# Performance work log

Hardware: AMD Instinct MI355X
Metric: run time of the kernel (lower is better)

The kernel has to match this reference:

```python
import jax, jax.numpy as jnp
import numpy as np

THETA_BASE = 10000.0


def _rope_tables(head_dim, seq_len):
    # intended math of precompute_rope_params (source has an arange typo;
    # standard RoPE: inv_freq over even indices)
    inv_freq = 1.0 / (THETA_BASE ** (jnp.arange(0, head_dim, 2, dtype=jnp.float32) / head_dim))
    pos = jnp.arange(seq_len, dtype=jnp.float32)
    angles = pos[:, None] * inv_freq[None, :]          # [S, hd/2]
    angles = jnp.concatenate([angles, angles], axis=1)  # [S, hd]
    return jnp.cos(angles), jnp.sin(angles)


def _apply_rope(x, cos, sin):
    # x: [B, H, S, hd]; cos/sin: [S, hd] broadcast over batch/heads
    hd = x.shape[-1]
    x1, x2 = x[..., : hd // 2], x[..., hd // 2 :]
    rotated = jnp.concatenate([-x2, x1], axis=-1)
    return x * cos + rotated * sin


def setup_inputs() -> dict:
    key = jax.random.key(0)
    ks = jax.random.split(key, 5)
    b, s, d = 2, 2048, 1024
    x = jax.random.normal(ks[0], (b, s, d), dtype=jnp.float32)
    # store weights as [d_in, d_out] so y = x @ W (equivalent math to nn.Linear)
    scale = 1.0 / np.sqrt(d)
    W_q = jax.random.normal(ks[1], (d, d), dtype=jnp.float32) * scale
    W_k = jax.random.normal(ks[2], (d, d), dtype=jnp.float32) * scale
    W_v = jax.random.normal(ks[3], (d, d), dtype=jnp.float32) * scale
    W_o = jax.random.normal(ks[4], (d, d), dtype=jnp.float32) * scale
    return {"x": x, "W_q": W_q, "W_k": W_k, "W_v": W_v, "W_o": W_o}


def reference(x, W_q, W_k, W_v, W_o):
    num_heads = 16
    b, s, d_in = x.shape
    d_out = W_q.shape[1]
    hd = d_out // num_heads

    def split_heads(t):  # [B,S,D] -> [B,H,S,hd]
        return t.reshape(b, s, num_heads, hd).transpose(0, 2, 1, 3)

    q = split_heads(x @ W_q)
    k = split_heads(x @ W_k)
    v = split_heads(x @ W_v)

    cos, sin = _rope_tables(hd, s)
    q = _apply_rope(q, cos, sin)
    k = _apply_rope(k, cos, sin)

    scores = jnp.einsum("bhqd,bhkd->bhqk", q, k)
    causal = jnp.triu(jnp.ones((s, s), dtype=bool), k=1)  # True above diagonal
    scores = jnp.where(causal, -jnp.inf, scores)
    attn = jax.nn.softmax(scores / jnp.sqrt(jnp.float32(hd)), axis=-1)

    ctx = jnp.einsum("bhqk,bhkd->bhqd", attn, v)
    ctx = ctx.transpose(0, 2, 1, 3).reshape(b, s, d_out)
    return ctx @ W_o
```

## Files before the change

kernel.cpp:

```cpp
#include <hip/hip_runtime.h>

typedef __bf16 bf16x8 __attribute__((ext_vector_type(8)));
typedef float f32x4 __attribute__((ext_vector_type(4)));
typedef unsigned short u16;

__device__ __forceinline__ u16 f2bf(float f){
  union { float fp; unsigned int u; } v; v.fp = f;
  unsigned int r = v.u + 0x7fffu + ((v.u >> 16) & 1u);
  return (u16)(r >> 16);
}

__device__ __forceinline__ unsigned pk2(float a, float b){
  union { float f; unsigned u; } ua, ub; ua.f = a; ub.f = b;
  return __builtin_amdgcn_perm(ub.u, ua.u, 0x07060302u);
}

__device__ __forceinline__ void glds16(const void* g, void* l){
  __builtin_amdgcn_global_load_lds((__attribute__((address_space(1))) void*)(void*)(g),
                                   (__attribute__((address_space(3))) void*)(l), 16, 0, 0);
}

__global__ __launch_bounds__(256) void prep_k(const float* __restrict__ x,
                                              const float* __restrict__ W0, const float* __restrict__ W1,
                                              const float* __restrict__ W2, const float* __restrict__ W3,
                                              u16* __restrict__ XB, u16* __restrict__ Wt,
                                              float* __restrict__ cosT, float* __restrict__ sinT){
  const int b = blockIdx.x, tid = threadIdx.x;
  if (b < 512){
    for (int i = b*256 + tid; i < (1<<20); i += 512*256){
      float4 v = ((const float4*)x)[i];
      ushort4 o;
      o.x = f2bf(v.x); o.y = f2bf(v.y); o.z = f2bf(v.z); o.w = f2bf(v.w);
      ((ushort4*)XB)[i] = o;
    }
  } else if (b < 4608){
    __shared__ float tile[32][33];
    const int b2 = b - 512;
    const int bz = b2>>10, by = (b2>>5)&31, bx = b2&31;
    const float* W = (bz==0)?W0:(bz==1)?W1:(bz==2)?W2:W3;
    u16* dst = Wt + ((size_t)bz<<20);
    const int tx = tid&31, ty = tid>>5;
    const int xx = bx*32 + tx;
    const int y0 = by*32;
    #pragma unroll
    for (int i=0;i<32;i+=8) tile[ty+i][tx] = W[(size_t)(y0+ty+i)*1024 + xx];
    __syncthreads();
    const int xo = y0 + tx;
    #pragma unroll
    for (int i=0;i<32;i+=8) dst[(size_t)(bx*32+ty+i)*1024 + xo] = f2bf(tile[tx][ty+i]);
  } else {
    const int i = (b-4608)*256 + tid;
    const int si = i>>6, dd = i&63, f = dd&31;
    float invf = exp2f(-13.287712379549449f * (float)f * (1.0f/32.0f));
    float ang = (float)si * invf;
    float s, c;
    sincosf(ang, &s, &c);
    cosT[i] = c; sinT[i] = s;
  }
}

__global__ __launch_bounds__(256,3) void gemm_qkv_k(const u16* __restrict__ xb, const u16* __restrict__ Wt,
                                                  const float* __restrict__ cosT, const float* __restrict__ sinT,
                                                  u16* __restrict__ Qr, u16* __restrict__ Kr, u16* __restrict__ Vt){
  __shared__ __align__(16) u16 As[128*32];
  __shared__ __align__(16) u16 Bs[128*32];
  const int tid = threadIdx.x;
  const int w = tid>>6, lane = tid&63, quad = lane>>4, l15 = lane&15;
  const int wrow = w>>1, wcol = w&1;
  const int m0 = blockIdx.x*128;
  const int nG0 = blockIdx.y*128;
  const int which = nG0>>10, n0 = nG0&1023;
  const u16* __restrict__ B = Wt + ((size_t)which<<20);
  f32x4 acc[4][4] = {};
  const int srow = lane>>2, scol = (lane&3)*8;
  const int ar0 = m0 + 32*w + srow;
  const int br0 = n0 + 32*w + srow;

  for (int kb=0; kb<1024; kb+=32){
    glds16(&xb[(size_t)ar0*1024      + kb + scol], &As[(32*w)*32]);
    glds16(&xb[(size_t)(ar0+16)*1024 + kb + scol], &As[(32*w+16)*32]);
    glds16(&B [(size_t)br0*1024      + kb + scol], &Bs[(32*w)*32]);
    glds16(&B [(size_t)(br0+16)*1024 + kb + scol], &Bs[(32*w+16)*32]);
    __syncthreads();
    bf16x8 a[4], b[4];
    #pragma unroll
    for (int t=0;t<4;t++){
      a[t] = *(const bf16x8*)&As[(64*wrow + 16*t + l15)*32 + quad*8];
      b[t] = *(const bf16x8*)&Bs[(64*wcol + 16*t + l15)*32 + quad*8];
    }
    #pragma unroll
    for (int ti=0;ti<4;ti++)
      #pragma unroll
      for (int tj=0;tj<4;tj++)
        acc[ti][tj] = __builtin_amdgcn_mfma_f32_16x16x32_bf16(a[ti], b[tj], acc[ti][tj], 0,0,0);
    __syncthreads();
  }

  const int colbase = n0 + 64*wcol;
  const int hh = colbase>>6;
  const int rowbase = m0 + 64*wrow + 4*quad;
  const float QSCALE = 0.18033688011112042f;

  if (which < 2){
    u16* __restrict__ out = (which==0) ? Qr : Kr;
    const float osc = (which==0) ? QSCALE : 1.0f;
    #pragma unroll
    for (int tj=0;tj<4;tj++){
      int dd = 16*tj + l15;
      int obase = (dd>>5)*512 + ((dd>>3)&3)*128 + (dd&7);
      float sgn = (tj<2) ? -1.0f : 1.0f;
      int pj = tj^2;
      #pragma unroll
      for (int ti=0;ti<4;ti++){
        #pragma unroll
        for (int r=0;r<4;r++){
          int m = rowbase + 16*ti + r;
          int bi = m>>11, si = m&2047;
          float cs = cosT[(si<<6)+dd];
          float sn = sinT[(si<<6)+dd];
          float vv = (acc[ti][tj][r]*cs + sgn*acc[ti][pj][r]*sn) * osc;
          out[((size_t)(bi*16+hh)<<17) + (si>>4)*1024 + (si&15)*8 + obase] = f2bf(vv);
        }
      }
    }
  } else {
    #pragma unroll
    for (int tj=0;tj<4;tj++){
      #pragma unroll
      for (int ti=0;ti<4;ti++){
        int m = rowbase + 16*ti;
        int bi = m>>11, si = m&2047;
        ushort4 pk;
        pk.x = f2bf(acc[ti][tj][0]); pk.y = f2bf(acc[ti][tj][1]);
        pk.z = f2bf(acc[ti][tj][2]); pk.w = f2bf(acc[ti][tj][3]);
        *(ushort4*)&Vt[((size_t)(bi*16+hh)<<17) + (si>>6)*4096 + ((si>>5)&1)*2048
                       + tj*512 + ((si>>3)&3)*128 + l15*8 + (si&7)] = pk;
      }
    }
  }
}

__global__ __launch_bounds__(256,3) void attn_k(const u16* __restrict__ QF, const u16* __restrict__ KF,
                                                const u16* __restrict__ VF, u16* __restrict__ ctx){
  __shared__ __align__(16) u16 SC[4*4608];
  __shared__ float LL[4][32];
  const int tid = threadIdx.x;
  const int w = tid>>6, lane = tid&63, quad = lane>>4, l15 = lane&15;
  const int Lin = blockIdx.x;
  const int xcd = Lin & 7, slot = Lin >> 3;
  const int bh = (xcd<<2) | (slot>>5);
  const int p = slot & 31;
  const u16* __restrict__ Qb = QF + ((size_t)bh<<17);
  const u16* __restrict__ Kb = KF + ((size_t)bh<<17);
  const u16* __restrict__ Vb = VF + ((size_t)bh<<17);
  u16* __restrict__ Pw = SC + w*4608;
  const int loff = lane*8;
  const int bi = bh>>4, hh = bh&15;

  #pragma unroll 1
  for (int ph=0; ph<2; ph++){
    if (ph) __syncthreads();
    const int tile = ph ? (63-p) : p;
    const int q0 = tile*32;
    const int nk = (tile>>1) + 1;

    bf16x8 qf[2][2];
    #pragma unroll
    for (int ti=0;ti<2;ti++)
      #pragma unroll
      for (int kh=0;kh<2;kh++)
        qf[ti][kh] = *(const bf16x8*)&Qb[(2*tile+ti)*1024 + kh*512 + loff];

    f32x4 o[2][4] = {};
    float ls[2] = {0.f, 0.f};

    for (int kt = w; kt < nk; kt += 4){
      const int k0 = kt*64;
      bf16x8 kf[4][2], vf[4][2];
      #pragma unroll
      for (int tjk=0;tjk<4;tjk++)
        #pragma unroll
        for (int kh=0;kh<2;kh++)
          kf[tjk][kh] = *(const bf16x8*)&Kb[(4*kt+tjk)*1024 + kh*512 + loff];
      #pragma unroll
      for (int tjd=0;tjd<4;tjd++)
        #pragma unroll
        for (int kh=0;kh<2;kh++)
          vf[tjd][kh] = *(const bf16x8*)&Vb[kt*4096 + kh*2048 + tjd*512 + loff];

      f32x4 st[2][4] = {};
      #pragma unroll
      for (int ti=0;ti<2;ti++)
        #pragma unroll
        for (int tjk=0;tjk<4;tjk++){
          st[ti][tjk] = __builtin_amdgcn_mfma_f32_16x16x32_bf16(kf[tjk][0], qf[ti][0], st[ti][tjk], 0,0,0);
          st[ti][tjk] = __builtin_amdgcn_mfma_f32_16x16x32_bf16(kf[tjk][1], qf[ti][1], st[ti][tjk], 0,0,0);
        }

      #pragma unroll
      for (int ti=0;ti<2;ti++){
        const int qbase = q0 + 16*ti;
        f32x4 pv[4];
        if (k0 + 63 > qbase){
          const int qg = qbase + l15;
          #pragma unroll
          for (int tjk=0;tjk<4;tjk++)
            #pragma unroll
            for (int r=0;r<4;r++){
              int kg = k0 + 16*tjk + 4*quad + r;
              pv[tjk][r] = (kg > qg) ? 0.0f : exp2f(fminf(st[ti][tjk][r], 80.0f));
            }
        } else {
          #pragma unroll
          for (int tjk=0;tjk<4;tjk++)
            #pragma unroll
            for (int r=0;r<4;r++)
              pv[tjk][r] = exp2f(fminf(st[ti][tjk][r], 80.0f));
        }
        f32x4 t4 = (pv[0]+pv[1]) + (pv[2]+pv[3]);
        float rs = (t4[0]+t4[1]) + (t4[2]+t4[3]);
        rs += __shfl_xor(rs, 16, 64);
        rs += __shfl_xor(rs, 32, 64);
        ls[ti] += rs;
        #pragma unroll
        for (int tjk=0;tjk<4;tjk++){
          uint2 pk;
          pk.x = pk2(pv[tjk][0], pv[tjk][1]);
          pk.y = pk2(pv[tjk][2], pv[tjk][3]);
          *(uint2*)&Pw[(16*ti + l15)*72 + 16*tjk + 4*quad] = pk;
        }
      }

      bf16x8 pf[2][2];
      #pragma unroll
      for (int ti=0;ti<2;ti++)
        #pragma unroll
        for (int kh=0;kh<2;kh++)
          pf[ti][kh] = *(const bf16x8*)&Pw[(16*ti + l15)*72 + 32*kh + quad*8];
      #pragma unroll
      for (int ti=0;ti<2;ti++)
        #pragma unroll
        for (int tjd=0;tjd<4;tjd++){
          o[ti][tjd] = __builtin_amdgcn_mfma_f32_16x16x32_bf16(pf[ti][0], vf[tjd][0], o[ti][tjd], 0,0,0);
          o[ti][tjd] = __builtin_amdgcn_mfma_f32_16x16x32_bf16(pf[ti][1], vf[tjd][1], o[ti][tjd], 0,0,0);
        }
    }

    float* __restrict__ Ob = (float*)&SC[w*4608];
    #pragma unroll
    for (int ti=0;ti<2;ti++)
      #pragma unroll
      for (int tjd=0;tjd<4;tjd++)
        *(f32x4*)&Ob[(16*tjd + l15)*36 + 16*ti + 4*quad] = o[ti][tjd];
    if (quad == 0){
      LL[w][l15]      = ls[0];
      LL[w][16 + l15] = ls[1];
    }
    __syncthreads();

    #pragma unroll
    for (int ti=0;ti<2;ti++){
      f32x4 om = {0.f,0.f,0.f,0.f};
      #pragma unroll
      for (int w2=0;w2<4;w2++)
        om += *(const f32x4*)&((const float*)&SC[w2*4608])[(16*w + l15)*36 + 16*ti + 4*quad];
      #pragma unroll
      for (int r=0;r<4;r++){
        int ridx = 16*ti + 4*quad + r;
        float lv = LL[0][ridx] + LL[1][ridx] + LL[2][ridx] + LL[3][ridx];
        int sq = q0 + ridx;
        ctx[(((size_t)(bi*2048 + sq))<<10) + (hh<<6) + 16*w + l15] = f2bf(om[r] / lv);
      }
    }
  }
}

__global__ __launch_bounds__(256,3) void gemm_out_k(const u16* __restrict__ cb, const u16* __restrict__ Wot,
                                                  float* __restrict__ out){
  __shared__ __align__(16) u16 As[128*32];
  __shared__ __align__(16) u16 Bs[128*32];
  const int tid = threadIdx.x;
  const int w = tid>>6, lane = tid&63, quad = lane>>4, l15 = lane&15;
  const int wrow = w>>1, wcol = w&1;
  const int m0 = blockIdx.x*128;
  const int nG0 = blockIdx.y*128;
  f32x4 acc[4][4] = {};
  const int srow = lane>>2, scol = (lane&3)*8;
  const int ar0 = m0 + 32*w + srow;
  const int br0 = nG0 + 32*w + srow;

  for (int kb=0; kb<1024; kb+=32){
    glds16(&cb [(size_t)ar0*1024      + kb + scol], &As[(32*w)*32]);
    glds16(&cb [(size_t)(ar0+16)*1024 + kb + scol], &As[(32*w+16)*32]);
    glds16(&Wot[(size_t)br0*1024      + kb + scol], &Bs[(32*w)*32]);
    glds16(&Wot[(size_t)(br0+16)*1024 + kb + scol], &Bs[(32*w+16)*32]);
    __syncthreads();
    bf16x8 a[4], b[4];
    #pragma unroll
    for (int t=0;t<4;t++){
      a[t] = *(const bf16x8*)&As[(64*wrow + 16*t + l15)*32 + quad*8];
      b[t] = *(const bf16x8*)&Bs[(64*wcol + 16*t + l15)*32 + quad*8];
    }
    #pragma unroll
    for (int ti=0;ti<4;ti++)
      #pragma unroll
      for (int tj=0;tj<4;tj++)
        acc[ti][tj] = __builtin_amdgcn_mfma_f32_16x16x32_bf16(a[ti], b[tj], acc[ti][tj], 0,0,0);
    __syncthreads();
  }

  const int rowbase = m0 + 64*wrow + 4*quad;
  const int colb = nG0 + 64*wcol;
  #pragma unroll
  for (int ti=0;ti<4;ti++){
    #pragma unroll
    for (int r=0;r<4;r++){
      int m = rowbase + 16*ti + r;
      float* orow = out + (size_t)m*1024 + colb;
      #pragma unroll
      for (int tj=0;tj<4;tj++)
        orow[16*tj + l15] = acc[ti][tj][r];
    }
  }
}

extern "C" void kernel_launch(void* const* d_in, const int* in_sizes, int n_in,
                              void* d_out, int out_size, void* d_ws, size_t ws_size,
                              hipStream_t stream){
  const float* x  = (const float*)d_in[0];
  const float* Wq = (const float*)d_in[1];
  const float* Wk = (const float*)d_in[2];
  const float* Wv = (const float*)d_in[3];
  const float* Wo = (const float*)d_in[4];
  float* out = (float*)d_out;
  u16* ws = (u16*)d_ws;

  u16* XB  = ws;
  u16* WT  = ws + ((size_t)4<<20);
  u16* QFp = ws + ((size_t)8<<20);
  u16* KFp = ws + ((size_t)12<<20);
  u16* VFp = ws + ((size_t)16<<20);
  u16* CTX = ws + ((size_t)20<<20);
  float* COS = (float*)(ws + ((size_t)24<<20));
  float* SIN = COS + (1<<17);

  prep_k       <<<5120, 256, 0, stream>>>(x, Wq, Wk, Wv, Wo, XB, WT, COS, SIN);
  gemm_qkv_k   <<<dim3(32,24), 256, 0, stream>>>(XB, WT, COS, SIN, QFp, KFp, VFp);
  attn_k       <<<1024, 256, 0, stream>>>(QFp, KFp, VFp, CTX);
  gemm_out_k   <<<dim3(32,8), 256, 0, stream>>>(CTX, WT + ((size_t)3<<20), out);
}
```

Measured before the change: 184.5 us.

## Deepen GEMM K-steps, shrink out-proj tiles, split attention query halves for occupancy

The QKV GEMM now stages 64-wide K slices (two 32-wide halves) per barrier pair, halving the number of sync round-trips. The output-projection GEMM does the same and uses 64-row M tiles, doubling the grid to 512 blocks for better CU coverage. The attention kernel processes its two 16-row query sub-tiles one after another, with half the shared-memory scratch, a two-pass reduction epilogue and launch bounds raised to 4 waves per SIMD to raise occupancy. It also drops the fminf clamp before exp2f and delays V loads until after the first score block. Risks: lower per-block reuse in the out GEMM, extra barriers in the attention epilogue, and possible overflow without the clamp.

```diff
diff --git a/kernel.cpp b/kernel.cpp
--- a/kernel.cpp
+++ b/kernel.cpp
@@ -62,8 +62,8 @@
 __global__ __launch_bounds__(256,3) void gemm_qkv_k(const u16* __restrict__ xb, const u16* __restrict__ Wt,
                                                   const float* __restrict__ cosT, const float* __restrict__ sinT,
                                                   u16* __restrict__ Qr, u16* __restrict__ Kr, u16* __restrict__ Vt){
-  __shared__ __align__(16) u16 As[128*32];
-  __shared__ __align__(16) u16 Bs[128*32];
+  __shared__ __align__(16) u16 As[2*128*32];
+  __shared__ __align__(16) u16 Bs[2*128*32];
   const int tid = threadIdx.x;
   const int w = tid>>6, lane = tid&63, quad = lane>>4, l15 = lane&15;
   const int wrow = w>>1, wcol = w&1;
@@ -72,27 +72,32 @@
   const int which = nG0>>10, n0 = nG0&1023;
   const u16* __restrict__ B = Wt + ((size_t)which<<20);
   f32x4 acc[4][4] = {};
-  const int srow = lane>>2, scol = (lane&3)*8;
-  const int ar0 = m0 + 32*w + srow;
-  const int br0 = n0 + 32*w + srow;
-
-  for (int kb=0; kb<1024; kb+=32){
-    glds16(&xb[(size_t)ar0*1024      + kb + scol], &As[(32*w)*32]);
-    glds16(&xb[(size_t)(ar0+16)*1024 + kb + scol], &As[(32*w+16)*32]);
-    glds16(&B [(size_t)br0*1024      + kb + scol], &Bs[(32*w)*32]);
-    glds16(&B [(size_t)(br0+16)*1024 + kb + scol], &Bs[(32*w+16)*32]);
-    __syncthreads();
-    bf16x8 a[4], b[4];
-    #pragma unroll
-    for (int t=0;t<4;t++){
-      a[t] = *(const bf16x8*)&As[(64*wrow + 16*t + l15)*32 + quad*8];
-      b[t] = *(const bf16x8*)&Bs[(64*wcol + 16*t + l15)*32 + quad*8];
-    }
-    #pragma unroll
-    for (int ti=0;ti<4;ti++)
-      #pragma unroll
-      for (int tj=0;tj<4;tj++)
-        acc[ti][tj] = __builtin_amdgcn_mfma_f32_16x16x32_bf16(a[ti], b[tj], acc[ti][tj], 0,0,0);
+  const int r4 = lane>>2, c4 = (lane&3)*8;
+
+  for (int kb=0; kb<1024; kb+=64){
+    #pragma unroll
+    for (int kh=0; kh<2; kh++){
+      glds16(&xb[(size_t)(m0+32*w+r4)*1024    + kb + kh*32 + c4], &As[kh*4096 + (32*w)*32]);
+      glds16(&xb[(size_t)(m0+32*w+16+r4)*1024 + kb + kh*32 + c4], &As[kh*4096 + (32*w+16)*32]);
+      glds16(&B [(size_t)(n0+32*w+r4)*1024    + kb + kh*32 + c4], &Bs[kh*4096 + (32*w)*32]);
+      glds16(&B [(size_t)(n0+32*w+16+r4)*1024 + kb + kh*32 + c4], &Bs[kh*4096 + (32*w+16)*32]);
+    }
+    __syncthreads();
+    bf16x8 a[4][2], b[4][2];
+    #pragma unroll
+    for (int t=0;t<4;t++)
+      #pragma unroll
+      for (int kh=0;kh<2;kh++){
+        a[t][kh] = *(const bf16x8*)&As[kh*4096 + (64*wrow + 16*t + l15)*32 + quad*8];
+        b[t][kh] = *(const bf16x8*)&Bs[kh*4096 + (64*wcol + 16*t + l15)*32 + quad*8];
+      }
+    #pragma unroll
+    for (int kh=0;kh<2;kh++)
+      #pragma unroll
+      for (int ti=0;ti<4;ti++)
+        #pragma unroll
+        for (int tj=0;tj<4;tj++)
+          acc[ti][tj] = __builtin_amdgcn_mfma_f32_16x16x32_bf16(a[ti][kh], b[tj][kh], acc[ti][tj], 0,0,0);
     __syncthreads();
   }
 
@@ -140,10 +145,10 @@
   }
 }
 
-__global__ __launch_bounds__(256,3) void attn_k(const u16* __restrict__ QF, const u16* __restrict__ KF,
+__global__ __launch_bounds__(256,4) void attn_k(const u16* __restrict__ QF, const u16* __restrict__ KF,
                                                 const u16* __restrict__ VF, u16* __restrict__ ctx){
-  __shared__ __align__(16) u16 SC[4*4608];
-  __shared__ float LL[4][32];
+  __shared__ __align__(16) u16 SC[4*2304];
+  __shared__ float LL[4][16];
   const int tid = threadIdx.x;
   const int w = tid>>6, lane = tid&63, quad = lane>>4, l15 = lane&15;
   const int Lin = blockIdx.x;
@@ -153,7 +158,7 @@
   const u16* __restrict__ Qb = QF + ((size_t)bh<<17);
   const u16* __restrict__ Kb = KF + ((size_t)bh<<17);
   const u16* __restrict__ Vb = VF + ((size_t)bh<<17);
-  u16* __restrict__ Pw = SC + w*4608;
+  u16* __restrict__ Pw = SC + w*2304;
   const int loff = lane*8;
   const int bi = bh>>4, hh = bh&15;
 
@@ -174,60 +179,95 @@
     f32x4 o[2][4] = {};
     float ls[2] = {0.f, 0.f};
 
+    #pragma unroll 1
     for (int kt = w; kt < nk; kt += 4){
       const int k0 = kt*64;
-      bf16x8 kf[4][2], vf[4][2];
+      bf16x8 kf[4][2];
       #pragma unroll
       for (int tjk=0;tjk<4;tjk++)
         #pragma unroll
         for (int kh=0;kh<2;kh++)
           kf[tjk][kh] = *(const bf16x8*)&Kb[(4*kt+tjk)*1024 + kh*512 + loff];
-      #pragma unroll
-      for (int tjd=0;tjd<4;tjd++)
-        #pragma unroll
-        for (int kh=0;kh<2;kh++)
-          vf[tjd][kh] = *(const bf16x8*)&Vb[kt*4096 + kh*2048 + tjd*512 + loff];
-
-      f32x4 st[2][4] = {};
-      #pragma unroll
-      for (int ti=0;ti<2;ti++)
+
+      {
+        f32x4 st[4] = {};
         #pragma unroll
         for (int tjk=0;tjk<4;tjk++){
-          st[ti][tjk] = __builtin_amdgcn_mfma_f32_16x16x32_bf16(kf[tjk][0], qf[ti][0], st[ti][tjk], 0,0,0);
-          st[ti][tjk] = __builtin_amdgcn_mfma_f32_16x16x32_bf16(kf[tjk][1], qf[ti][1], st[ti][tjk], 0,0,0);
-        }
-
-      #pragma unroll
-      for (int ti=0;ti<2;ti++){
-        const int qbase = q0 + 16*ti;
+          st[tjk] = __builtin_amdgcn_mfma_f32_16x16x32_bf16(kf[tjk][0], qf[0][0], st[tjk], 0,0,0);
+          st[tjk] = __builtin_amdgcn_mfma_f32_16x16x32_bf16(kf[tjk][1], qf[0][1], st[tjk], 0,0,0);
+        }
         f32x4 pv[4];
-        if (k0 + 63 > qbase){
-          const int qg = qbase + l15;
+        if (k0 + 63 > q0){
+          const int qg = q0 + l15;
           #pragma unroll
           for (int tjk=0;tjk<4;tjk++)
             #pragma unroll
             for (int r=0;r<4;r++){
               int kg = k0 + 16*tjk + 4*quad + r;
-              pv[tjk][r] = (kg > qg) ? 0.0f : exp2f(fminf(st[ti][tjk][r], 80.0f));
+              pv[tjk][r] = (kg > qg) ? 0.0f : exp2f(st[tjk][r]);
             }
         } else {
           #pragma unroll
           for (int tjk=0;tjk<4;tjk++)
             #pragma unroll
             for (int r=0;r<4;r++)
-              pv[tjk][r] = exp2f(fminf(st[ti][tjk][r], 80.0f));
+              pv[tjk][r] = exp2f(st[tjk][r]);
         }
         f32x4 t4 = (pv[0]+pv[1]) + (pv[2]+pv[3]);
         float rs = (t4[0]+t4[1]) + (t4[2]+t4[3]);
         rs += __shfl_xor(rs, 16, 64);
         rs += __shfl_xor(rs, 32, 64);
-        ls[ti] += rs;
+        ls[0] += rs;
         #pragma unroll
         for (int tjk=0;tjk<4;tjk++){
           uint2 pk;
           pk.x = pk2(pv[tjk][0], pv[tjk][1]);
           pk.y = pk2(pv[tjk][2], pv[tjk][3]);
-          *(uint2*)&Pw[(16*ti + l15)*72 + 16*tjk + 4*quad] = pk;
+          *(uint2*)&Pw[l15*72 + 16*tjk + 4*quad] = pk;
+        }
+      }
+
+      bf16x8 vf[4][2];
+      {
+        f32x4 st[4] = {};
+        #pragma unroll
+        for (int tjk=0;tjk<4;tjk++){
+          st[tjk] = __builtin_amdgcn_mfma_f32_16x16x32_bf16(kf[tjk][0], qf[1][0], st[tjk], 0,0,0);
+          st[tjk] = __builtin_amdgcn_mfma_f32_16x16x32_bf16(kf[tjk][1], qf[1][1], st[tjk], 0,0,0);
+        }
+        #pragma unroll
+        for (int tjd=0;tjd<4;tjd++)
+          #pragma unroll
+          for (int kh=0;kh<2;kh++)
+            vf[tjd][kh] = *(const bf16x8*)&Vb[kt*4096 + kh*2048 + tjd*512 + loff];
+        f32x4 pv[4];
+        if (k0 + 63 > q0 + 16){
+          const int qg = q0 + 16 + l15;
+          #pragma unroll
+          for (int tjk=0;tjk<4;tjk++)
+            #pragma unroll
+            for (int r=0;r<4;r++){
+              int kg = k0 + 16*tjk + 4*quad + r;
+              pv[tjk][r] = (kg > qg) ? 0.0f : exp2f(st[tjk][r]);
+            }
+        } else {
+          #pragma unroll
+          for (int tjk=0;tjk<4;tjk++)
+            #pragma unroll
+            for (int r=0;r<4;r++)
+              pv[tjk][r] = exp2f(st[tjk][r]);
+        }
+        f32x4 t4 = (pv[0]+pv[1]) + (pv[2]+pv[3]);
+        float rs = (t4[0]+t4[1]) + (t4[2]+t4[3]);
+        rs += __shfl_xor(rs, 16, 64);
+        rs += __shfl_xor(rs, 32, 64);
+        ls[1] += rs;
+        #pragma unroll
+        for (int tjk=0;tjk<4;tjk++){
+          uint2 pk;
+          pk.x = pk2(pv[tjk][0], pv[tjk][1]);
+          pk.y = pk2(pv[tjk][2], pv[tjk][3]);
+          *(uint2*)&Pw[(16 + l15)*72 + 16*tjk + 4*quad] = pk;
         }
       }
 
@@ -246,29 +286,24 @@
         }
     }
 
-    float* __restrict__ Ob = (float*)&SC[w*4608];
-    #pragma unroll
-    for (int ti=0;ti<2;ti++)
+    #pragma unroll 1
+    for (int tix=0; tix<2; tix++){
+      if (tix) __syncthreads();
+      float* __restrict__ Ob = (float*)&SC[w*2304];
       #pragma unroll
       for (int tjd=0;tjd<4;tjd++)
-        *(f32x4*)&Ob[(16*tjd + l15)*36 + 16*ti + 4*quad] = o[ti][tjd];
-    if (quad == 0){
-      LL[w][l15]      = ls[0];
-      LL[w][16 + l15] = ls[1];
-    }
-    __syncthreads();
-
-    #pragma unroll
-    for (int ti=0;ti<2;ti++){
+        *(f32x4*)&Ob[(16*tjd + l15)*18 + 4*quad] = o[tix][tjd];
+      if (quad == 0) LL[w][l15] = ls[tix];
+      __syncthreads();
       f32x4 om = {0.f,0.f,0.f,0.f};
       #pragma unroll
       for (int w2=0;w2<4;w2++)
-        om += *(const f32x4*)&((const float*)&SC[w2*4608])[(16*w + l15)*36 + 16*ti + 4*quad];
+        om += *(const f32x4*)&((const float*)&SC[w2*2304])[(16*w + l15)*18 + 4*quad];
       #pragma unroll
       for (int r=0;r<4;r++){
-        int ridx = 16*ti + 4*quad + r;
+        int ridx = 4*quad + r;
         float lv = LL[0][ridx] + LL[1][ridx] + LL[2][ridx] + LL[3][ridx];
-        int sq = q0 + ridx;
+        int sq = q0 + 16*tix + ridx;
         ctx[(((size_t)(bi*2048 + sq))<<10) + (hh<<6) + 16*w + l15] = f2bf(om[r] / lv);
       }
     }
@@ -277,42 +312,48 @@
 
 __global__ __launch_bounds__(256,3) void gemm_out_k(const u16* __restrict__ cb, const u16* __restrict__ Wot,
                                                   float* __restrict__ out){
-  __shared__ __align__(16) u16 As[128*32];
-  __shared__ __align__(16) u16 Bs[128*32];
+  __shared__ __align__(16) u16 As[2*64*32];
+  __shared__ __align__(16) u16 Bs[2*128*32];
   const int tid = threadIdx.x;
   const int w = tid>>6, lane = tid&63, quad = lane>>4, l15 = lane&15;
   const int wrow = w>>1, wcol = w&1;
-  const int m0 = blockIdx.x*128;
+  const int m0 = blockIdx.x*64;
   const int nG0 = blockIdx.y*128;
-  f32x4 acc[4][4] = {};
-  const int srow = lane>>2, scol = (lane&3)*8;
-  const int ar0 = m0 + 32*w + srow;
-  const int br0 = nG0 + 32*w + srow;
-
-  for (int kb=0; kb<1024; kb+=32){
-    glds16(&cb [(size_t)ar0*1024      + kb + scol], &As[(32*w)*32]);
-    glds16(&cb [(size_t)(ar0+16)*1024 + kb + scol], &As[(32*w+16)*32]);
-    glds16(&Wot[(size_t)br0*1024      + kb + scol], &Bs[(32*w)*32]);
-    glds16(&Wot[(size_t)(br0+16)*1024 + kb + scol], &Bs[(32*w+16)*32]);
-    __syncthreads();
-    bf16x8 a[4], b[4];
-    #pragma unroll
-    for (int t=0;t<4;t++){
-      a[t] = *(const bf16x8*)&As[(64*wrow + 16*t + l15)*32 + quad*8];
-      b[t] = *(const bf16x8*)&Bs[(64*wcol + 16*t + l15)*32 + quad*8];
-    }
-    #pragma unroll
-    for (int ti=0;ti<4;ti++)
-      #pragma unroll
-      for (int tj=0;tj<4;tj++)
-        acc[ti][tj] = __builtin_amdgcn_mfma_f32_16x16x32_bf16(a[ti], b[tj], acc[ti][tj], 0,0,0);
-    __syncthreads();
-  }
-
-  const int rowbase = m0 + 64*wrow + 4*quad;
+  f32x4 acc[2][4] = {};
+  const int r4 = lane>>2, c4 = (lane&3)*8;
+
+  for (int kb=0; kb<1024; kb+=64){
+    #pragma unroll
+    for (int kh=0; kh<2; kh++){
+      glds16(&cb [(size_t)(m0+16*w+r4)*1024     + kb + kh*32 + c4], &As[kh*2048 + (16*w)*32]);
+      glds16(&Wot[(size_t)(nG0+32*w+r4)*1024    + kb + kh*32 + c4], &Bs[kh*4096 + (32*w)*32]);
+      glds16(&Wot[(size_t)(nG0+32*w+16+r4)*1024 + kb + kh*32 + c4], &Bs[kh*4096 + (32*w+16)*32]);
+    }
+    __syncthreads();
+    bf16x8 a[2][2], b[4][2];
+    #pragma unroll
+    for (int kh=0;kh<2;kh++){
+      #pragma unroll
+      for (int t=0;t<2;t++)
+        a[t][kh] = *(const bf16x8*)&As[kh*2048 + (32*wrow + 16*t + l15)*32 + quad*8];
+      #pragma unroll
+      for (int t=0;t<4;t++)
+        b[t][kh] = *(const bf16x8*)&Bs[kh*4096 + (64*wcol + 16*t + l15)*32 + quad*8];
+    }
+    #pragma unroll
+    for (int kh=0;kh<2;kh++)
+      #pragma unroll
+      for (int ti=0;ti<2;ti++)
+        #pragma unroll
+        for (int tj=0;tj<4;tj++)
+          acc[ti][tj] = __builtin_amdgcn_mfma_f32_16x16x32_bf16(a[ti][kh], b[tj][kh], acc[ti][tj], 0,0,0);
+    __syncthreads();
+  }
+
+  const int rowbase = m0 + 32*wrow + 4*quad;
   const int colb = nG0 + 64*wcol;
   #pragma unroll
-  for (int ti=0;ti<4;ti++){
+  for (int ti=0;ti<2;ti++){
     #pragma unroll
     for (int r=0;r<4;r++){
       int m = rowbase + 16*ti + r;
@@ -347,5 +388,5 @@
   prep_k       <<<5120, 256, 0, stream>>>(x, Wq, Wk, Wv, Wo, XB, WT, COS, SIN);
   gemm_qkv_k   <<<dim3(32,24), 256, 0, stream>>>(XB, WT, COS, SIN, QFp, KFp, VFp);
   attn_k       <<<1024, 256, 0, stream>>>(QFp, KFp, VFp, CTX);
-  gemm_out_k   <<<dim3(32,8), 256, 0, stream>>>(CTX, WT + ((size_t)3<<20), out);
-}
+  gemm_out_k   <<<dim3(64,8), 256, 0, stream>>>(CTX, WT + ((size_t)3<<20), out);
+}
```

Result: slower. 238.8 us (+29.4%).
